# Kernel tuning notes

Measured on AMD Instinct MI355X. Metric: run time of the kernel, lower is better.

The kernel has to match this reference:

```python
import jax, jax.numpy as jnp
import numpy as np

N = 65536      # total nodes
B = 128        # graphs in batch
NP = 512       # nodes per graph (N = B*NP)
E = 524288     # edges, avg degree 8, kept within-graph
DIN = 128      # input feature dim
C = 256        # hidden channels
H = 4          # attention heads
DH = C // H
EPS_NRM = 1e-12  # F.normalize eps (SAGEConv normalize=True)
EPS = 1e-5       # GraphNorm / LayerNorm eps


def _xavier(k, shape):
    lim = np.sqrt(6.0 / (shape[-1] + shape[-2]))
    return jax.random.uniform(k, shape, jnp.float32, -lim, lim)


def setup_inputs() -> dict:
    key = jax.random.key(0)
    ks = jax.random.split(key, 20)
    g = jnp.arange(E) // (E // B)  # graph id per edge
    src = (jax.random.randint(ks[0], (E,), 0, NP) + g * NP).astype(jnp.int32)
    dst = (jax.random.randint(ks[1], (E,), 0, NP) + g * NP).astype(jnp.int32)
    edge_index = jnp.stack([src, dst])
    batch = (jnp.arange(N) // NP).astype(jnp.int32)
    x = jax.random.normal(ks[2], (N, DIN), jnp.float32)
    return dict(
        x=x, edge_index=edge_index, batch=batch,
        l0_lin_l_w=_xavier(ks[3], (C, DIN)), l0_lin_l_b=jnp.zeros((C,), jnp.float32),
        l0_lin_r_w=_xavier(ks[4], (C, DIN)),
        l0_res_w=_xavier(ks[5], (C, DIN)),
        lin_l_w=jnp.stack([_xavier(ks[6 + i], (C, C)) for i in range(3)]),
        lin_l_b=jnp.zeros((3, C), jnp.float32),
        lin_r_w=jnp.stack([_xavier(ks[9 + i], (C, C)) for i in range(3)]),
        gn_w=jnp.ones((4, C), jnp.float32), gn_b=jnp.zeros((4, C), jnp.float32),
        gn_alpha=jnp.ones((4, C), jnp.float32),
        attn_in_w=_xavier(ks[12], (3 * C, C)), attn_in_b=jnp.zeros((3 * C,), jnp.float32),
        attn_out_w=_xavier(ks[13], (C, C)), attn_out_b=jnp.zeros((C,), jnp.float32),
        ln_w=jnp.ones((C,), jnp.float32), ln_b=jnp.zeros((C,), jnp.float32),
        pool_w=_xavier(ks[14], (C, 3 * C)), pool_b=jnp.zeros((C,), jnp.float32),
    )


def _forward(x, src, dst, batch, p):
    (l0_lin_l_w, l0_lin_l_b, l0_lin_r_w, l0_res_w, lin_l_w, lin_l_b, lin_r_w,
     gn_w, gn_b, gn_alpha, attn_in_w, attn_in_b, attn_out_w, attn_out_b,
     ln_w, ln_b, pool_w, pool_b) = p
    gelu = lambda v: jax.nn.gelu(v, approximate=False)  # torch nn.GELU default (erf)
    deg = jnp.maximum(jax.ops.segment_sum(jnp.ones((E,), x.dtype), dst, num_segments=N), 1.0)[:, None]

    def sage(h, w_l, b_l, w_r):
        # SAGEConv(mean aggr, normalize=True): lin_l(mean_j x_j) + lin_r(x_i), then L2-normalize
        agg = jax.ops.segment_sum(h[src], dst, num_segments=N) / deg
        out = agg @ w_l.T + b_l + h @ w_r.T
        return out / jnp.maximum(jnp.linalg.norm(out, axis=-1, keepdims=True), EPS_NRM)

    def graph_norm(h, w, b, alpha):
        # GraphNorm: w * (h - alpha*mean_g) / sqrt(var_g + eps) + b, per-graph per-channel
        mean = (jax.ops.segment_sum(h, batch, num_segments=B) / NP)[batch]
        out = h - alpha * mean
        var = (jax.ops.segment_sum(out * out, batch, num_segments=B) / NP)[batch]
        return w * out / jnp.sqrt(var + EPS) + b

    # GNN blocks (eval mode: dropout = identity); layer 0 has residual projection DIN->C
    h = gelu(graph_norm(sage(x, l0_lin_l_w, l0_lin_l_b, l0_lin_r_w), gn_w[0], gn_b[0], gn_alpha[0]))
    x1 = h + x @ l0_res_w.T
    for i in range(3):
        h = gelu(graph_norm(sage(x1, lin_l_w[i], lin_l_b[i], lin_r_w[i]), gn_w[i + 1], gn_b[i + 1], gn_alpha[i + 1]))
        x1 = h + x1

    # BatchedAttentionBlock: equal-size graphs -> to_dense_batch is a reshape, mask all-true
    xd = x1.reshape(B, NP, C)
    qkv = xd @ attn_in_w.T + attn_in_b
    q, k, v = jnp.split(qkv, 3, axis=-1)
    to_h = lambda t: t.reshape(B, NP, H, DH).transpose(0, 2, 1, 3)
    q, k, v = to_h(q), to_h(k), to_h(v)
    scores = jnp.einsum('bhqd,bhkd->bhqk', q, k) / np.float32(np.sqrt(DH))
    attn = jax.nn.softmax(scores, axis=-1)
    o = jnp.einsum('bhqk,bhkd->bhqd', attn, v).transpose(0, 2, 1, 3).reshape(B, NP, C)
    o = o @ attn_out_w.T + attn_out_b
    x2 = o.reshape(N, C) + x1

    # LayerNorm(mode='graph'): normalize over all nodes*features of each graph
    xg = x2.reshape(B, NP * C)
    mu = xg.mean(axis=1, keepdims=True)
    cen = xg - mu
    var = (cen * cen).mean(axis=1, keepdims=True)
    x3 = gelu((cen / jnp.sqrt(var + EPS)).reshape(N, C) * ln_w + ln_b)

    # multi-pool (mean/max/sum) + projection -> graph embedding [B, C]
    xp = x3.reshape(B, NP, C)
    pooled = jnp.concatenate([xp.mean(1), xp.max(1), xp.sum(1)], axis=1)
    return pooled @ pool_w.T + pool_b


def reference(x, edge_index, batch, l0_lin_l_w, l0_lin_l_b, l0_lin_r_w, l0_res_w,
              lin_l_w, lin_l_b, lin_r_w, gn_w, gn_b, gn_alpha,
              attn_in_w, attn_in_b, attn_out_w, attn_out_b, ln_w, ln_b, pool_w, pool_b):
    src, dst = edge_index[0], edge_index[1]
    p = (l0_lin_l_w, l0_lin_l_b, l0_lin_r_w, l0_res_w, lin_l_w, lin_l_b, lin_r_w,
         gn_w, gn_b, gn_alpha, attn_in_w, attn_in_b, attn_out_w, attn_out_b,
         ln_w, ln_b, pool_w, pool_b)
    return _forward(x, src, dst, batch, p)
```

## Files before the change

kernel.cpp:

```cpp
#include <hip/hip_runtime.h>


#define N_TOT   65536
#define B_GR    128
#define NP_     512
#define E_TOT   524288
#define EPG     4096
#define DIN_    128
#define C_      256
#define C3_     768
#define H_      4

typedef unsigned int uint;
typedef unsigned short ushort;

#define O_L0LW  0u
#define O_L0LB  32768u
#define O_L0RW  33024u
#define O_L0RES 65792u
#define O_LWL   98560u
#define O_LBL   295168u
#define O_LWR   295936u
#define O_GNW   492544u
#define O_GNB   493568u
#define O_GNA   494592u
#define O_AIW   495616u
#define O_AIB   692224u
#define O_AOW   692992u
#define O_AOB   758528u
#define O_LNW   758784u
#define O_LNB   759040u
#define O_PLW   759296u
#define O_PLB   955904u
#define TOTALP  956160u

typedef __attribute__((ext_vector_type(8))) short bf16x8_t;
typedef __attribute__((ext_vector_type(4))) float f32x4_t;

__device__ __forceinline__ float bf2f(ushort u){ union{uint i; float f;} v; v.i = ((uint)u) << 16; return v.f; }
__device__ __forceinline__ ushort f2bf(float f){
  union{float f; uint u;} v; v.f = f;
  uint u = v.u;
  u += 0x7fffu + ((u >> 16) & 1u);
  return (ushort)(u >> 16);
}
__device__ __forceinline__ uint pack2(float a, float b){ return (uint)f2bf(a) | ((uint)f2bf(b) << 16); }
__device__ __forceinline__ float u2f_lo(uint u){ union{uint i; float f;} v; v.i = u << 16; return v.f; }
__device__ __forceinline__ float u2f_hi(uint u){ union{uint i; float f;} v; v.i = u & 0xffff0000u; return v.f; }
__device__ __forceinline__ float gelu_f(float x){ return 0.5f * x * (1.0f + erff(x * 0.70710678118654752440f)); }
__device__ __forceinline__ float wredsum(float v){
  #pragma unroll
  for (int off = 32; off; off >>= 1) v += __shfl_xor(v, off, 64);
  return v;
}

__global__ void probe_dtype(const uint* __restrict__ gnw_raw, uint* __restrict__ flag){
  if (threadIdx.x == 0 && blockIdx.x == 0)
    *flag = (gnw_raw[0] == 0x3F800000u) ? 1u : 0u;
}

struct Seg { const void* p; uint ofs; };
struct CvtArgs { Seg s[19]; };

__global__ __launch_bounds__(256) void cvt_params(CvtArgs a, ushort* __restrict__ pb,
                                                  const uint* __restrict__ flag){
  uint gi = blockIdx.x * 256u + threadIdx.x;
  if (gi >= TOTALP) return;
  int lo = 0;
  #pragma unroll
  for (int s = 1; s < 18; ++s) if (gi >= a.s[s].ofs) lo = s;
  uint rel = gi - a.s[lo].ofs;
  pb[gi] = (*flag) ? f2bf(((const float*)a.s[lo].p)[rel]) : ((const ushort*)a.s[lo].p)[rel];
}

__global__ __launch_bounds__(256) void cvt_flat(const void* __restrict__ in, ushort* __restrict__ out,
                                                const uint* __restrict__ flag){
  uint i = blockIdx.x * 256u + threadIdx.x;
  out[i] = (*flag) ? f2bf(((const float*)in)[i]) : ((const ushort*)in)[i];
}

__global__ void deg_count(const int* __restrict__ dst, uint* __restrict__ deg){
  int e = blockIdx.x * 256 + threadIdx.x;
  atomicAdd(&deg[dst[e]], 1u);
}

__global__ __launch_bounds__(512) void scan_deg(const uint* __restrict__ deg,
    uint* __restrict__ rowptr, uint* __restrict__ cursor)
{
  __shared__ uint s[512];
  const int g = blockIdx.x, tid = threadIdx.x;
  uint v = deg[g * NP_ + tid];
  s[tid] = v;
  __syncthreads();
  #pragma unroll
  for (int off = 1; off < 512; off <<= 1) {
    uint t = (tid >= off) ? s[tid - off] : 0u;
    __syncthreads();
    s[tid] += t;
    __syncthreads();
  }
  uint p = g * EPG + (s[tid] - v);
  rowptr[g * NP_ + tid] = p;
  cursor[g * NP_ + tid] = p;
}

__global__ void scatter_edges(const int* __restrict__ src, const int* __restrict__ dst,
    uint* __restrict__ cursor, int* __restrict__ csr)
{
  int e = blockIdx.x * 256 + threadIdx.x;
  uint p = atomicAdd(&cursor[dst[e]], 1u);
  csr[p] = src[e];
}

template<int D>
__global__ __launch_bounds__(256) void sage_agg_csr(const ushort* __restrict__ X,
    const int* __restrict__ csr, const uint* __restrict__ rowptr,
    const uint* __restrict__ deg, ushort* __restrict__ agg)
{
  constexpr int CPL = D / 64;
  const int tid = threadIdx.x, lane = tid & 63, wave = tid >> 6;
  const int n = blockIdx.x * 4 + wave;
  const uint start = rowptr[n];
  const uint dg = deg[n];
  const int co = lane * CPL;
  float acc[CPL];
  #pragma unroll
  for (int k = 0; k < CPL; ++k) acc[k] = 0.0f;

  auto addrow = [&](int s) {
    const ushort* r = X + (size_t)s * D + co;
    if constexpr (CPL == 2) {
      uint u = *(const uint*)r;
      acc[0] += u2f_lo(u); acc[1] += u2f_hi(u);
    } else {
      uint2 u = *(const uint2*)r;
      acc[0] += u2f_lo(u.x); acc[1] += u2f_hi(u.x);
      acc[2] += u2f_lo(u.y); acc[3] += u2f_hi(u.y);
    }
  };

  uint j = 0;
  for (; j + 4 <= dg; j += 4) {
    int s0 = csr[start + j],     s1 = csr[start + j + 1];
    int s2 = csr[start + j + 2], s3 = csr[start + j + 3];
    addrow(s0); addrow(s1); addrow(s2); addrow(s3);
  }
  for (; j < dg; ++j) addrow(csr[start + j]);

  float inv = 1.0f / (float)(dg < 1u ? 1u : dg);
  ushort* op = agg + (size_t)n * D + co;
  if constexpr (CPL == 2) {
    *(uint*)op = pack2(acc[0] * inv, acc[1] * inv);
  } else {
    uint2 o; o.x = pack2(acc[0] * inv, acc[1] * inv);
    o.y = pack2(acc[2] * inv, acc[3] * inv);
    *(uint2*)op = o;
  }
}

#define CS_P 260
template<bool DUAL, bool RN>
__global__ __launch_bounds__(256, 4) void gemm_mfma(
    const ushort* __restrict__ A1, int lda1, const ushort* __restrict__ W1,
    const ushort* __restrict__ A2, int lda2, const ushort* __restrict__ W2,
    const ushort* __restrict__ bias, const ushort* addend,
    ushort* out, int K, int ldOut,
    float* __restrict__ m1, float* __restrict__ m2)
{
  __shared__ __align__(16) unsigned char smem[34816];
  ushort* As = (ushort*)smem;
  float*  Cs = (float*)smem;
  const int tid = threadIdx.x;
  const int lane = tid & 63, wave = tid >> 6;
  const int lr = lane & 15, quad = lane >> 4;
  const int m0 = blockIdx.x * 64;
  const int n0b = blockIdx.y * 256;
  const int n0 = n0b + wave * 64;
  const int KP = K + 8;
  f32x4_t acc[4][4];
  #pragma unroll
  for (int rt = 0; rt < 4; ++rt)
    #pragma unroll
    for (int ct = 0; ct < 4; ++ct) acc[rt][ct] = (f32x4_t){0.f, 0.f, 0.f, 0.f};

  const int lpr = K >> 3;
  const int rpp = 256 / lpr;
  const int passes = 64 / rpp;
  const int tr = tid / lpr, tc = (tid % lpr) * 8;

  for (int p = 0; p < passes; ++p) {
    int row = p * rpp + tr;
    *(bf16x8_t*)(As + row * KP + tc) =
        *(const bf16x8_t*)(A1 + (size_t)(m0 + row) * lda1 + tc);
  }
  __syncthreads();
  {
    const ushort* wp = W1 + (size_t)(n0 + lr) * K + quad * 8;
    for (int kb = 0; kb < K; kb += 32) {
      bf16x8_t a[4], b[4];
      #pragma unroll
      for (int ct = 0; ct < 4; ++ct) b[ct] = *(const bf16x8_t*)(wp + (size_t)(ct * 16) * K + kb);
      #pragma unroll
      for (int rt = 0; rt < 4; ++rt)
        a[rt] = *(const bf16x8_t*)(As + (rt * 16 + lr) * KP + kb + quad * 8);
      #pragma unroll
      for (int rt = 0; rt < 4; ++rt)
        #pragma unroll
        for (int ct = 0; ct < 4; ++ct)
          acc[rt][ct] = __builtin_amdgcn_mfma_f32_16x16x32_bf16(a[rt], b[ct], acc[rt][ct], 0, 0, 0);
    }
  }
  __syncthreads();
  if constexpr (DUAL) {
    for (int p = 0; p < passes; ++p) {
      int row = p * rpp + tr;
      *(bf16x8_t*)(As + row * KP + tc) =
          *(const bf16x8_t*)(A2 + (size_t)(m0 + row) * lda2 + tc);
    }
    __syncthreads();
    const ushort* wp = W2 + (size_t)(n0 + lr) * K + quad * 8;
    for (int kb = 0; kb < K; kb += 32) {
      bf16x8_t a[4], b[4];
      #pragma unroll
      for (int ct = 0; ct < 4; ++ct) b[ct] = *(const bf16x8_t*)(wp + (size_t)(ct * 16) * K + kb);
      #pragma unroll
      for (int rt = 0; rt < 4; ++rt)
        a[rt] = *(const bf16x8_t*)(As + (rt * 16 + lr) * KP + kb + quad * 8);
      #pragma unroll
      for (int rt = 0; rt < 4; ++rt)
        #pragma unroll
        for (int ct = 0; ct < 4; ++ct)
          acc[rt][ct] = __builtin_amdgcn_mfma_f32_16x16x32_bf16(a[rt], b[ct], acc[rt][ct], 0, 0, 0);
    }
    __syncthreads();
  }

  float bvs[4];
  if (RN && bias) {
    #pragma unroll
    for (int ct = 0; ct < 4; ++ct) bvs[ct] = bf2f(bias[n0 + ct * 16 + lr]);
  }
  float bvL[4] = {0.f, 0.f, 0.f, 0.f};
  if (!RN && bias) {
    #pragma unroll
    for (int j = 0; j < 4; ++j) bvL[j] = bf2f(bias[n0b + lane * 4 + j]);
  }
  float a1s[4] = {0.f, 0.f, 0.f, 0.f}, a2s[4] = {0.f, 0.f, 0.f, 0.f};
  #pragma unroll
  for (int round = 0; round < 2; ++round) {
    #pragma unroll
    for (int rt2 = 0; rt2 < 2; ++rt2) {
      int rt = round * 2 + rt2;
      #pragma unroll
      for (int ct = 0; ct < 4; ++ct)
        #pragma unroll
        for (int r = 0; r < 4; ++r) {
          float v = acc[rt][ct][r];
          if constexpr (RN) v += bias ? bvs[ct] : 0.0f;
          Cs[(rt2 * 16 + quad * 4 + r) * CS_P + wave * 64 + ct * 16 + lr] = v;
        }
    }
    __syncthreads();
    #pragma unroll
    for (int it = 0; it < 8; ++it) {
      int row = wave * 8 + it;
      float4 v = *(const float4*)(Cs + row * CS_P + lane * 4);
      int grow = m0 + round * 32 + row;
      size_t ob = (size_t)grow * ldOut + n0b + lane * 4;
      if constexpr (RN) {
        float ss = v.x*v.x + v.y*v.y + v.z*v.z + v.w*v.w;
        ss = wredsum(ss);
        float inv = 1.0f / fmaxf(sqrtf(ss), 1e-12f);
        float r0 = v.x * inv, r1 = v.y * inv, r2 = v.z * inv, r3 = v.w * inv;
        a1s[0] += r0; a1s[1] += r1; a1s[2] += r2; a1s[3] += r3;
        a2s[0] += r0*r0; a2s[1] += r1*r1; a2s[2] += r2*r2; a2s[3] += r3*r3;
        uint2 o; o.x = pack2(r0, r1); o.y = pack2(r2, r3);
        *(uint2*)(out + ob) = o;
      } else {
        float r0 = v.x + bvL[0], r1 = v.y + bvL[1], r2 = v.z + bvL[2], r3 = v.w + bvL[3];
        if (addend) {
          uint2 ad = *(const uint2*)(addend + ob);
          r0 += u2f_lo(ad.x); r1 += u2f_hi(ad.x);
          r2 += u2f_lo(ad.y); r3 += u2f_hi(ad.y);
        }
        uint2 o; o.x = pack2(r0, r1); o.y = pack2(r2, r3);
        *(uint2*)(out + ob) = o;
      }
    }
    __syncthreads();
  }
  if constexpr (RN) {
    const int g = m0 >> 9;
    #pragma unroll
    for (int k = 0; k < 4; ++k) {
      atomicAdd(&m1[g*C_ + lane * 4 + k], a1s[k]);
      atomicAdd(&m2[g*C_ + lane * 4 + k], a2s[k]);
    }
  }
}

__global__ __launch_bounds__(256) void gn_gelu_add(const ushort* __restrict__ h,
    const ushort* res,
    const float* __restrict__ m1, const float* __restrict__ m2,
    const ushort* __restrict__ gw, const ushort* __restrict__ gb, const ushort* __restrict__ ga,
    ushort* out)
{
  size_t b4 = ((size_t)blockIdx.x * 256 + threadIdx.x) * 4;
  int c = (int)(b4 & (C_ - 1));
  int n = (int)(b4 >> 8);
  int g = n >> 9;
  uint2 hv = *(const uint2*)(h + b4);
  uint2 rv = *(const uint2*)(res + b4);
  float hh[4] = {u2f_lo(hv.x), u2f_hi(hv.x), u2f_lo(hv.y), u2f_hi(hv.y)};
  float rr[4] = {u2f_lo(rv.x), u2f_hi(rv.x), u2f_lo(rv.y), u2f_hi(rv.y)};
  float oo[4];
  #pragma unroll
  for (int j = 0; j < 4; ++j) {
    int cc = c + j;
    float a  = bf2f(ga[cc]);
    float mm = m1[g*C_ + cc] * (1.0f / 512.0f);
    float q2 = m2[g*C_ + cc] * (1.0f / 512.0f);
    float var = q2 - a * (2.0f - a) * mm * mm;
    float xo = hh[j] - a * mm;
    float y = bf2f(gw[cc]) * xo * rsqrtf(var + 1e-5f) + bf2f(gb[cc]);
    oo[j] = gelu_f(y) + rr[j];
  }
  uint2 ov; ov.x = pack2(oo[0], oo[1]); ov.y = pack2(oo[2], oo[3]);
  *(uint2*)(out + b4) = ov;
}

#define KS_P 72
#define VT_P 520
#define PW_P 40
__global__ __launch_bounds__(512, 2) void attn_kernel(ushort* __restrict__ qkv)
{
  __shared__ ushort Ks[NP_ * KS_P];
  __shared__ ushort Vt[64 * VT_P];
  __shared__ ushort Pw[8][16 * PW_P];
  const int bid = blockIdx.x;
  const int g = bid >> 2, h = bid & 3;
  const int tid = threadIdx.x, lane = tid & 63, wave = tid >> 6;
  const int lr = lane & 15, quad = lane >> 4;
  const size_t base = (size_t)g * NP_ * C3_;
  const int qoff = h * 64, koff = C_ + h * 64, voff = 2 * C_ + h * 64;
  for (int idx = tid; idx < NP_ * 64; idx += 512) {
    int j = idx >> 6, c = idx & 63;
    const ushort* row = qkv + base + (size_t)j * C3_;
    Ks[j * KS_P + c] = row[koff + c];
    Vt[c * VT_P + j] = row[voff + c];
  }
  __syncthreads();
  ushort* pw = &Pw[wave][0];
  const int q0 = wave * 64;
  for (int qt = 0; qt < 4; ++qt) {
    const int qr = q0 + qt * 16;
    const ushort* qp = qkv + base + (size_t)(qr + lr) * C3_ + qoff + quad * 8;
    bf16x8_t qa0 = *(const bf16x8_t*)(qp);
    bf16x8_t qa1 = *(const bf16x8_t*)(qp + 32);
    f32x4_t s[32];
    #pragma unroll
    for (int t = 0; t < 32; ++t) {
      const ushort* kp = Ks + (size_t)(t * 16 + lr) * KS_P + quad * 8;
      bf16x8_t b0 = *(const bf16x8_t*)(kp);
      bf16x8_t b1 = *(const bf16x8_t*)(kp + 32);
      f32x4_t a = (f32x4_t){0.f, 0.f, 0.f, 0.f};
      a = __builtin_amdgcn_mfma_f32_16x16x32_bf16(qa0, b0, a, 0, 0, 0);
      a = __builtin_amdgcn_mfma_f32_16x16x32_bf16(qa1, b1, a, 0, 0, 0);
      s[t] = a;
    }
    float invv[4];
    #pragma unroll
    for (int r = 0; r < 4; ++r) {
      float m = s[0][r];
      #pragma unroll
      for (int t = 1; t < 32; ++t) m = fmaxf(m, s[t][r]);
      #pragma unroll
      for (int off = 8; off; off >>= 1) m = fmaxf(m, __shfl_xor(m, off, 64));
      float sm = 0.0f;
      #pragma unroll
      for (int t = 0; t < 32; ++t) {
        float e = __expf((s[t][r] - m) * 0.125f);
        s[t][r] = e; sm += e;
      }
      #pragma unroll
      for (int off = 8; off; off >>= 1) sm += __shfl_xor(sm, off, 64);
      invv[r] = 1.0f / sm;
    }
    f32x4_t o[4];
    #pragma unroll
    for (int t = 0; t < 4; ++t) o[t] = (f32x4_t){0.f, 0.f, 0.f, 0.f};
    for (int kc = 0; kc < 16; ++kc) {
      #pragma unroll
      for (int half = 0; half < 2; ++half) {
        int t = kc * 2 + half;
        #pragma unroll
        for (int r = 0; r < 4; ++r)
          pw[(quad * 4 + r) * PW_P + half * 16 + lr] = f2bf(s[t][r] * invv[r]);
      }
      __threadfence_block();
      bf16x8_t pa = *(const bf16x8_t*)(pw + lr * PW_P + quad * 8);
      #pragma unroll
      for (int nt = 0; nt < 4; ++nt) {
        const ushort* vp = Vt + (size_t)(nt * 16 + lr) * VT_P + kc * 32 + quad * 8;
        bf16x8_t b = *(const bf16x8_t*)(vp);
        o[nt] = __builtin_amdgcn_mfma_f32_16x16x32_bf16(pa, b, o[nt], 0, 0, 0);
      }
    }
    #pragma unroll
    for (int nt = 0; nt < 4; ++nt)
      #pragma unroll
      for (int r = 0; r < 4; ++r)
        qkv[base + (size_t)(qr + quad * 4 + r) * C3_ + koff + nt * 16 + lr] =
            f2bf(o[nt][r]);
  }
}

__global__ __launch_bounds__(256) void ln_part(const ushort* __restrict__ x2, float* __restrict__ st2)
{
  __shared__ float a1[4], a2[4];
  const int g = blockIdx.x, sl = blockIdx.y;
  const int tid = threadIdx.x, lane = tid & 63, wave = tid >> 6;
  const ushort* p = x2 + ((size_t)g * NP_ + sl * 64) * C_;
  float s = 0.0f, q = 0.0f;
  for (int i = tid; i < 64 * C_; i += 256) { float v = bf2f(p[i]); s += v; q += v * v; }
  s = wredsum(s); q = wredsum(q);
  if (lane == 0) { a1[wave] = s; a2[wave] = q; }
  __syncthreads();
  if (tid == 0) {
    st2[(g * 8 + sl) * 2]     = a1[0] + a1[1] + a1[2] + a1[3];
    st2[(g * 8 + sl) * 2 + 1] = a2[0] + a2[1] + a2[2] + a2[3];
  }
}

__global__ __launch_bounds__(256) void ln_gelu(const ushort* __restrict__ x2, const float* __restrict__ st2,
    const ushort* __restrict__ lw, const ushort* __restrict__ lb, ushort* __restrict__ x3)
{
  __shared__ float musd[2];
  size_t b4 = ((size_t)blockIdx.x * 256 + threadIdx.x) * 4;
  int c = (int)(b4 & (C_ - 1));
  int g = (int)(b4 >> 17);
  if (threadIdx.x == 0) {
    float S = 0.0f, Q = 0.0f;
    #pragma unroll
    for (int sl = 0; sl < 8; ++sl) {
      S += st2[(g * 8 + sl) * 2];
      Q += st2[(g * 8 + sl) * 2 + 1];
    }
    float mu = S * (1.0f / (NP_ * C_));
    float var = Q * (1.0f / (NP_ * C_)) - mu * mu;
    musd[0] = mu; musd[1] = rsqrtf(var + 1e-5f);
  }
  __syncthreads();
  float mu = musd[0], rs = musd[1];
  uint2 v = *(const uint2*)(x2 + b4);
  float vv[4] = {u2f_lo(v.x), u2f_hi(v.x), u2f_lo(v.y), u2f_hi(v.y)};
  float oo[4];
  #pragma unroll
  for (int j = 0; j < 4; ++j) {
    int cc = c + j;
    float y = (vv[j] - mu) * rs * bf2f(lw[cc]) + bf2f(lb[cc]);
    oo[j] = gelu_f(y);
  }
  uint2 ov; ov.x = pack2(oo[0], oo[1]); ov.y = pack2(oo[2], oo[3]);
  *(uint2*)(x3 + b4) = ov;
}

__global__ __launch_bounds__(256) void pool_part(const ushort* __restrict__ x3,
    float* __restrict__ psum, float* __restrict__ pmax)
{
  const int g = blockIdx.x, sl = blockIdx.y, c = threadIdx.x;
  const ushort* p = x3 + ((size_t)g * NP_ + sl * 64) * C_ + c;
  float s = 0.0f, mx = -3.0e38f;
  #pragma unroll 4
  for (int r = 0; r < 64; ++r) {
    float v = bf2f(p[(size_t)r * C_]);
    s += v; mx = fmaxf(mx, v);
  }
  psum[((size_t)g * 8 + sl) * C_ + c] = s;
  pmax[((size_t)g * 8 + sl) * C_ + c] = mx;
}

__global__ __launch_bounds__(256) void final_gemm(const float* __restrict__ psum,
    const float* __restrict__ pmax,
    const ushort* __restrict__ W, const ushort* __restrict__ b, void* __restrict__ out,
    const uint* __restrict__ flag)
{
  __shared__ float pl[C3_];
  const int g = blockIdx.x, c = threadIdx.x;
  float s = 0.0f, mx = -3.0e38f;
  #pragma unroll
  for (int sl = 0; sl < 8; ++sl) {
    s += psum[((size_t)g * 8 + sl) * C_ + c];
    mx = fmaxf(mx, pmax[((size_t)g * 8 + sl) * C_ + c]);
  }
  pl[c] = s * (1.0f / 512.0f);
  pl[C_ + c] = mx;
  pl[2 * C_ + c] = s;
  __syncthreads();
  float acc = bf2f(b[c]);
  const ushort* wr = W + (size_t)c * C3_;
  for (int k = 0; k < C3_; k += 2) {
    uint wv = *(const uint*)(wr + k);
    acc += pl[k] * u2f_lo(wv) + pl[k + 1] * u2f_hi(wv);
  }
  if (*flag) ((float*)out)[g * C_ + c] = acc;
  else       ((ushort*)out)[g * C_ + c] = f2bf(acc);
}

extern "C" void kernel_launch(void* const* d_in, const int* in_sizes, int n_in,
                              void* d_out, int out_size, void* d_ws, size_t ws_size,
                              hipStream_t stream)
{
  const int* ei   = (const int*)d_in[1];
  const int* srcp = ei;
  const int* dstp = ei + E_TOT;

  const size_t NC = (size_t)N_TOT * C_;
  const size_t NEEDED = (4ull << 20) + 4 * NC * sizeof(ushort);
  if (ws_size < NEEDED) return;

  unsigned char* wsb = (unsigned char*)d_ws;
  uint*   deg    = (uint*)wsb;
  float*  mbuf   = (float*)(wsb + (256u << 10));
  float*  st2    = (float*)(wsb + (1280u << 10));
  uint*   flag   = (uint*)(wsb + (1288u << 10));
  ushort* PB     = (ushort*)(wsb + (1792u << 10));
  ushort* S0     = (ushort*)(wsb + (4u << 20));
  ushort* S1     = S0 + NC;
  ushort* S2     = S1 + NC;
  ushort* S3     = S2 + NC;
  ushort* qkvb   = S1;
  ushort* XB     = S3;
  unsigned char* s3hi = (unsigned char*)(S3 + (size_t)N_TOT * DIN_);
  int*  csr    = (int*)s3hi;
  uint* rowptr = (uint*)(s3hi + (2u << 20));
  uint* cursor = (uint*)(s3hi + (2u << 20) + (256u << 10));
  float* psum  = (float*)S2;
  float* pmax  = psum + (size_t)B_GR * 8 * C_;

  probe_dtype<<<1, 1, 0, stream>>>((const uint*)d_in[10], flag);
  CvtArgs ca;
  ca.s[0]  = { d_in[3],  O_L0LW };  ca.s[1]  = { d_in[4],  O_L0LB };
  ca.s[2]  = { d_in[5],  O_L0RW };  ca.s[3]  = { d_in[6],  O_L0RES };
  ca.s[4]  = { d_in[7],  O_LWL  };  ca.s[5]  = { d_in[8],  O_LBL  };
  ca.s[6]  = { d_in[9],  O_LWR  };  ca.s[7]  = { d_in[10], O_GNW  };
  ca.s[8]  = { d_in[11], O_GNB  };  ca.s[9]  = { d_in[12], O_GNA  };
  ca.s[10] = { d_in[13], O_AIW  };  ca.s[11] = { d_in[14], O_AIB  };
  ca.s[12] = { d_in[15], O_AOW  };  ca.s[13] = { d_in[16], O_AOB  };
  ca.s[14] = { d_in[17], O_LNW  };  ca.s[15] = { d_in[18], O_LNB  };
  ca.s[16] = { d_in[19], O_PLW  };  ca.s[17] = { d_in[20], O_PLB  };
  ca.s[18] = { nullptr,  TOTALP };
  cvt_params<<<(TOTALP + 255) / 256, 256, 0, stream>>>(ca, PB, flag);
  cvt_flat<<<(N_TOT * DIN_) / 256, 256, 0, stream>>>(d_in[0], XB, flag);

  hipMemsetAsync(deg, 0, N_TOT * sizeof(uint), stream);
  hipMemsetAsync(mbuf, 0, (1u << 20), stream);

  deg_count<<<E_TOT / 256, 256, 0, stream>>>(dstp, deg);
  scan_deg<<<B_GR, 512, 0, stream>>>(deg, rowptr, cursor);
  scatter_edges<<<E_TOT / 256, 256, 0, stream>>>(srcp, dstp, cursor, csr);

  const size_t MSZ = (size_t)B_GR * C_;
  {
    float* m1 = mbuf;
    float* m2 = mbuf + MSZ * 4;
    sage_agg_csr<DIN_><<<N_TOT / 4, 256, 0, stream>>>(XB, csr, rowptr, deg, S1);
    gemm_mfma<true, true><<<dim3(N_TOT / 64, 1), 256, 0, stream>>>(
        S1, DIN_, PB + O_L0LW, XB, DIN_, PB + O_L0RW, PB + O_L0LB, nullptr, S2, DIN_, C_, m1, m2);
    gemm_mfma<false, false><<<dim3(N_TOT / 64, 1), 256, 0, stream>>>(
        XB, DIN_, PB + O_L0RES, nullptr, 0, nullptr, nullptr, nullptr, S0, DIN_, C_, nullptr, nullptr);
    gn_gelu_add<<<(N_TOT * C_) / 1024, 256, 0, stream>>>(S2, S0, m1, m2,
        PB + O_GNW, PB + O_GNB, PB + O_GNA, S0);
  }

  for (int i = 0; i < 3; ++i) {
    float* m1 = mbuf + MSZ * (i + 1);
    float* m2 = mbuf + MSZ * 4 + MSZ * (i + 1);
    sage_agg_csr<C_><<<N_TOT / 4, 256, 0, stream>>>(S0, csr, rowptr, deg, S1);
    gemm_mfma<true, true><<<dim3(N_TOT / 64, 1), 256, 0, stream>>>(
        S1, C_, PB + O_LWL + (size_t)i * C_ * C_, S0, C_, PB + O_LWR + (size_t)i * C_ * C_,
        PB + O_LBL + i * C_, nullptr, S2, C_, C_, m1, m2);
    gn_gelu_add<<<(N_TOT * C_) / 1024, 256, 0, stream>>>(S2, S0, m1, m2,
        PB + O_GNW + (i + 1) * C_, PB + O_GNB + (i + 1) * C_, PB + O_GNA + (i + 1) * C_, S0);
  }

  gemm_mfma<false, false><<<dim3(N_TOT / 64, 3), 256, 0, stream>>>(
      S0, C_, PB + O_AIW, nullptr, 0, nullptr, PB + O_AIB, nullptr, qkvb, C_, C3_, nullptr, nullptr);
  attn_kernel<<<B_GR * H_, 512, 0, stream>>>(qkvb);
  gemm_mfma<false, false><<<dim3(N_TOT / 64, 1), 256, 0, stream>>>(
      qkvb + C_, C3_, PB + O_AOW, nullptr, 0, nullptr, PB + O_AOB, S0, S0, C_, C_, nullptr, nullptr);

  ln_part<<<dim3(B_GR, 8), 256, 0, stream>>>(S0, st2);
  ln_gelu<<<(N_TOT * C_) / 1024, 256, 0, stream>>>(S0, st2, PB + O_LNW, PB + O_LNB, S1);

  pool_part<<<dim3(B_GR, 8), 256, 0, stream>>>(S1, psum, pmax);
  final_gemm<<<B_GR, 256, 0, stream>>>(psum, pmax, PB + O_PLW, PB + O_PLB, d_out, flag);
}
```

Before: 1.026 ms.

## Fuse LayerNorm statistics into out-projection GEMM and swizzle attention V tile

The per-graph sum and sum-of-squares for the graph LayerNorm are now accumulated in the attention out-projection GEMM epilogue and written with atomics into st2, so the separate ln_part kernel and its re-read of the activation tensor go away. The memset is enlarged to zero st2, which must sit right after mbuf. Separately, the transposed V tile in shared memory is XOR-swizzled to reduce LDS bank conflicts on the PV MFMA loads. The stats are taken from unrounded fp32 values instead of stored bf16, and atomic ordering makes the sums slightly non-deterministic.

```diff
diff --git a/kernel.cpp b/kernel.cpp
--- a/kernel.cpp
+++ b/kernel.cpp
@@ -159,13 +159,13 @@
 }
 
 #define CS_P 260
-template<bool DUAL, bool RN>
+template<bool DUAL, bool RN, bool LN>
 __global__ __launch_bounds__(256, 4) void gemm_mfma(
     const ushort* __restrict__ A1, int lda1, const ushort* __restrict__ W1,
     const ushort* __restrict__ A2, int lda2, const ushort* __restrict__ W2,
     const ushort* __restrict__ bias, const ushort* addend,
     ushort* out, int K, int ldOut,
-    float* __restrict__ m1, float* __restrict__ m2)
+    float* __restrict__ m1, float* __restrict__ m2, float* __restrict__ st2)
 {
   __shared__ __align__(16) unsigned char smem[34816];
   ushort* As = (ushort*)smem;
@@ -246,6 +246,7 @@
     for (int j = 0; j < 4; ++j) bvL[j] = bf2f(bias[n0b + lane * 4 + j]);
   }
   float a1s[4] = {0.f, 0.f, 0.f, 0.f}, a2s[4] = {0.f, 0.f, 0.f, 0.f};
+  float sln = 0.0f, qln = 0.0f;
   #pragma unroll
   for (int round = 0; round < 2; ++round) {
     #pragma unroll
@@ -283,6 +284,10 @@
           r0 += u2f_lo(ad.x); r1 += u2f_hi(ad.x);
           r2 += u2f_lo(ad.y); r3 += u2f_hi(ad.y);
         }
+        if constexpr (LN) {
+          sln += r0 + r1 + r2 + r3;
+          qln += r0*r0 + r1*r1 + r2*r2 + r3*r3;
+        }
         uint2 o; o.x = pack2(r0, r1); o.y = pack2(r2, r3);
         *(uint2*)(out + ob) = o;
       }
@@ -295,6 +300,14 @@
     for (int k = 0; k < 4; ++k) {
       atomicAdd(&m1[g*C_ + lane * 4 + k], a1s[k]);
       atomicAdd(&m2[g*C_ + lane * 4 + k], a2s[k]);
+    }
+  }
+  if constexpr (LN) {
+    const int g = m0 >> 9;
+    sln = wredsum(sln); qln = wredsum(qln);
+    if (lane == 0) {
+      atomicAdd(&st2[g * 2], sln);
+      atomicAdd(&st2[g * 2 + 1], qln);
     }
   }
 }
@@ -332,6 +345,7 @@
 #define KS_P 72
 #define VT_P 520
 #define PW_P 40
+__device__ __forceinline__ int vswz(int c){ return ((c >> 3) & 7) << 3; }
 __global__ __launch_bounds__(512, 2) void attn_kernel(ushort* __restrict__ qkv)
 {
   __shared__ ushort Ks[NP_ * KS_P];
@@ -347,7 +361,7 @@
     int j = idx >> 6, c = idx & 63;
     const ushort* row = qkv + base + (size_t)j * C3_;
     Ks[j * KS_P + c] = row[koff + c];
-    Vt[c * VT_P + j] = row[voff + c];
+    Vt[c * VT_P + (j ^ vswz(c))] = row[voff + c];
   }
   __syncthreads();
   ushort* pw = &Pw[wave][0];
@@ -401,7 +415,8 @@
       bf16x8_t pa = *(const bf16x8_t*)(pw + lr * PW_P + quad * 8);
       #pragma unroll
       for (int nt = 0; nt < 4; ++nt) {
-        const ushort* vp = Vt + (size_t)(nt * 16 + lr) * VT_P + kc * 32 + quad * 8;
+        int vrow = nt * 16 + lr;
+        const ushort* vp = Vt + (size_t)vrow * VT_P + ((kc * 32 + quad * 8) ^ vswz(vrow));
         bf16x8_t b = *(const bf16x8_t*)(vp);
         o[nt] = __builtin_amdgcn_mfma_f32_16x16x32_bf16(pa, b, o[nt], 0, 0, 0);
       }
@@ -412,23 +427,6 @@
       for (int r = 0; r < 4; ++r)
         qkv[base + (size_t)(qr + quad * 4 + r) * C3_ + koff + nt * 16 + lr] =
             f2bf(o[nt][r]);
-  }
-}
-
-__global__ __launch_bounds__(256) void ln_part(const ushort* __restrict__ x2, float* __restrict__ st2)
-{
-  __shared__ float a1[4], a2[4];
-  const int g = blockIdx.x, sl = blockIdx.y;
-  const int tid = threadIdx.x, lane = tid & 63, wave = tid >> 6;
-  const ushort* p = x2 + ((size_t)g * NP_ + sl * 64) * C_;
-  float s = 0.0f, q = 0.0f;
-  for (int i = tid; i < 64 * C_; i += 256) { float v = bf2f(p[i]); s += v; q += v * v; }
-  s = wredsum(s); q = wredsum(q);
-  if (lane == 0) { a1[wave] = s; a2[wave] = q; }
-  __syncthreads();
-  if (tid == 0) {
-    st2[(g * 8 + sl) * 2]     = a1[0] + a1[1] + a1[2] + a1[3];
-    st2[(g * 8 + sl) * 2 + 1] = a2[0] + a2[1] + a2[2] + a2[3];
   }
 }
 
@@ -440,12 +438,7 @@
   int c = (int)(b4 & (C_ - 1));
   int g = (int)(b4 >> 17);
   if (threadIdx.x == 0) {
-    float S = 0.0f, Q = 0.0f;
-    #pragma unroll
-    for (int sl = 0; sl < 8; ++sl) {
-      S += st2[(g * 8 + sl) * 2];
-      Q += st2[(g * 8 + sl) * 2 + 1];
-    }
+    float S = st2[g * 2], Q = st2[g * 2 + 1];
     float mu = S * (1.0f / (NP_ * C_));
     float var = Q * (1.0f / (NP_ * C_)) - mu * mu;
     musd[0] = mu; musd[1] = rsqrtf(var + 1e-5f);
@@ -554,7 +547,7 @@
   cvt_flat<<<(N_TOT * DIN_) / 256, 256, 0, stream>>>(d_in[0], XB, flag);
 
   hipMemsetAsync(deg, 0, N_TOT * sizeof(uint), stream);
-  hipMemsetAsync(mbuf, 0, (1u << 20), stream);
+  hipMemsetAsync(mbuf, 0, (1u << 20) + 1024, stream);
 
   deg_count<<<E_TOT / 256, 256, 0, stream>>>(dstp, deg);
   scan_deg<<<B_GR, 512, 0, stream>>>(deg, rowptr, cursor);
@@ -565,10 +558,10 @@
     float* m1 = mbuf;
     float* m2 = mbuf + MSZ * 4;
     sage_agg_csr<DIN_><<<N_TOT / 4, 256, 0, stream>>>(XB, csr, rowptr, deg, S1);
-    gemm_mfma<true, true><<<dim3(N_TOT / 64, 1), 256, 0, stream>>>(
-        S1, DIN_, PB + O_L0LW, XB, DIN_, PB + O_L0RW, PB + O_L0LB, nullptr, S2, DIN_, C_, m1, m2);
-    gemm_mfma<false, false><<<dim3(N_TOT / 64, 1), 256, 0, stream>>>(
-        XB, DIN_, PB + O_L0RES, nullptr, 0, nullptr, nullptr, nullptr, S0, DIN_, C_, nullptr, nullptr);
+    gemm_mfma<true, true, false><<<dim3(N_TOT / 64, 1), 256, 0, stream>>>(
+        S1, DIN_, PB + O_L0LW, XB, DIN_, PB + O_L0RW, PB + O_L0LB, nullptr, S2, DIN_, C_, m1, m2, nullptr);
+    gemm_mfma<false, false, false><<<dim3(N_TOT / 64, 1), 256, 0, stream>>>(
+        XB, DIN_, PB + O_L0RES, nullptr, 0, nullptr, nullptr, nullptr, S0, DIN_, C_, nullptr, nullptr, nullptr);
     gn_gelu_add<<<(N_TOT * C_) / 1024, 256, 0, stream>>>(S2, S0, m1, m2,
         PB + O_GNW, PB + O_GNB, PB + O_GNA, S0);
   }
@@ -577,20 +570,19 @@
     float* m1 = mbuf + MSZ * (i + 1);
     float* m2 = mbuf + MSZ * 4 + MSZ * (i + 1);
     sage_agg_csr<C_><<<N_TOT / 4, 256, 0, stream>>>(S0, csr, rowptr, deg, S1);
-    gemm_mfma<true, true><<<dim3(N_TOT / 64, 1), 256, 0, stream>>>(
+    gemm_mfma<true, true, false><<<dim3(N_TOT / 64, 1), 256, 0, stream>>>(
         S1, C_, PB + O_LWL + (size_t)i * C_ * C_, S0, C_, PB + O_LWR + (size_t)i * C_ * C_,
-        PB + O_LBL + i * C_, nullptr, S2, C_, C_, m1, m2);
+        PB + O_LBL + i * C_, nullptr, S2, C_, C_, m1, m2, nullptr);
     gn_gelu_add<<<(N_TOT * C_) / 1024, 256, 0, stream>>>(S2, S0, m1, m2,
         PB + O_GNW + (i + 1) * C_, PB + O_GNB + (i + 1) * C_, PB + O_GNA + (i + 1) * C_, S0);
   }
 
-  gemm_mfma<false, false><<<dim3(N_TOT / 64, 3), 256, 0, stream>>>(
-      S0, C_, PB + O_AIW, nullptr, 0, nullptr, PB + O_AIB, nullptr, qkvb, C_, C3_, nullptr, nullptr);
+  gemm_mfma<false, false, false><<<dim3(N_TOT / 64, 3), 256, 0, stream>>>(
+      S0, C_, PB + O_AIW, nullptr, 0, nullptr, PB + O_AIB, nullptr, qkvb, C_, C3_, nullptr, nullptr, nullptr);
   attn_kernel<<<B_GR * H_, 512, 0, stream>>>(qkvb);
-  gemm_mfma<false, false><<<dim3(N_TOT / 64, 1), 256, 0, stream>>>(
-      qkvb + C_, C3_, PB + O_AOW, nullptr, 0, nullptr, PB + O_AOB, S0, S0, C_, C_, nullptr, nullptr);
-
-  ln_part<<<dim3(B_GR, 8), 256, 0, stream>>>(S0, st2);
+  gemm_mfma<false, false, true><<<dim3(N_TOT / 64, 1), 256, 0, stream>>>(
+      qkvb + C_, C3_, PB + O_AOW, nullptr, 0, nullptr, PB + O_AOB, S0, S0, C_, C_, nullptr, nullptr, st2);
+
   ln_gelu<<<(N_TOT * C_) / 1024, 256, 0, stream>>>(S0, st2, PB + O_LNW, PB + O_LNB, S1);
 
   pool_part<<<dim3(B_GR, 8), 256, 0, stream>>>(S1, psum, pmax);
```

After: 1.021 ms. No clear change (-0.4%).
